# Kernel tuning notes

Measured on AMD Instinct MI355X. Metric: run time of the kernel, lower is better.

Reference implementation:

```python
import jax, jax.numpy as jnp
import numpy as np

B, M, T, N = 128, 256, 512, 512

def setup_inputs() -> dict:
    key = jax.random.key(0)
    ks = jax.random.split(key, 6)
    return {
        "hidden_state": jax.random.normal(ks[0], (B, M), jnp.float32),
        "cell_state": jax.random.normal(ks[1], (B, M), jnp.float32),
        "X": jax.random.normal(ks[2], (B, T, N), jnp.float32),
        "We1": jax.random.normal(ks[3], (2 * M, T), jnp.float32) * 0.05,
        "be1": jnp.zeros((T,), jnp.float32),
        "We2": jax.random.normal(ks[4], (T, T), jnp.float32) * 0.05,
        "be2": jnp.zeros((T,), jnp.float32),
        "v": jax.random.normal(ks[5], (T, 1), jnp.float32) * 0.05,
        "bv": jnp.zeros((1,), jnp.float32),
    }

def reference(hidden_state, cell_state, X, We1, be1, We2, be2, v, bv):
    # concat hidden + cell: [B, 2m]; Dense(T) then broadcast over n (K.repeat)
    hc = jnp.concatenate([hidden_state, cell_state], axis=-1)
    hs = (hc @ We1 + be1)[:, None, :]                 # [B, 1, T] (broadcast over n)
    # Permute X -> [B, n, T], Dense(T): contract over T
    ux = jnp.einsum('btn,tk->bnk', X, We2) + be2      # [B, n, T]
    # add + tanh + Dense(1) fused chain
    e = jnp.tanh(hs + ux) @ v + bv                    # [B, n, 1]
    # Permute -> [B, 1, n], softmax over last axis (n)
    attn = jax.nn.softmax(jnp.swapaxes(e, 1, 2), axis=-1)  # [B, 1, n]
    return attn
```

## Files before the change

kernel.cpp:

```cpp
#include <hip/hip_runtime.h>
#include <hip/hip_bf16.h>


typedef _Float16 half8 __attribute__((ext_vector_type(8)));
typedef float floatx4 __attribute__((ext_vector_type(4)));

__device__ __forceinline__ float fast_tanh(float x) {
    float cx = fminf(15.0f, fmaxf(-15.0f, x));
    float e = __expf(2.0f * cx);
    return (e - 1.0f) * __fdividef(1.0f, e + 1.0f);
}

__global__ __launch_bounds__(256) void k_prep_a(const float* __restrict__ We2,
                                                _Float16* __restrict__ Af) {
    __shared__ float w2[32][512];
    const int ts = blockIdx.x;
    for (int idx = threadIdx.x; idx < 32 * 512; idx += 256) {
        int tl = idx >> 9, k = idx & 511;
        w2[tl][k] = We2[(ts * 32 + tl) * 512 + k];
    }
    __syncthreads();
    for (int item = threadIdx.x; item < 32 * 64; item += 256) {
        int c = item >> 6, l = item & 63;
        int k  = c * 16 + (l & 15);
        int tl = (l >> 4) * 8;
        half8 h;
#pragma unroll
        for (int j = 0; j < 8; ++j) h[j] = (_Float16)w2[tl + j][k];
        *(half8*)&Af[(((size_t)ts * 32 + c) * 64 + l) * 8] = h;
    }
}

__global__ __launch_bounds__(256) void k_hs(const float* __restrict__ hidden,
                                            const float* __restrict__ cell,
                                            const float* __restrict__ We1,
                                            const float* __restrict__ be1,
                                            const float* __restrict__ be2,
                                            float* __restrict__ g) {
    __shared__ __align__(16) float hcl[8][512];
    __shared__ float red[4][8][64];
    const int b0 = (blockIdx.x >> 3) << 3;
    const int k0 = (blockIdx.x & 7) << 6;
    for (int idx = threadIdx.x; idx < 8 * 512; idx += 256) {
        int bi = idx >> 9, j = idx & 511;
        hcl[bi][j] = (j < 256) ? hidden[(b0 + bi) * 256 + j]
                               : cell[(b0 + bi) * 256 + j - 256];
    }
    __syncthreads();
    const int kl = threadIdx.x & 63;
    const int jc = threadIdx.x >> 6;
    const int k  = k0 + kl;
    float acc[8] = {};
    for (int j = jc * 128; j < jc * 128 + 128; j += 4) {
        float w0 = We1[(j + 0) * 512 + k];
        float w1 = We1[(j + 1) * 512 + k];
        float w2 = We1[(j + 2) * 512 + k];
        float w3 = We1[(j + 3) * 512 + k];
#pragma unroll
        for (int bi = 0; bi < 8; ++bi) {
            float4 h = *(const float4*)&hcl[bi][j];
            acc[bi] += h.x * w0 + h.y * w1 + h.z * w2 + h.w * w3;
        }
    }
#pragma unroll
    for (int bi = 0; bi < 8; ++bi) red[jc][bi][kl] = acc[bi];
    __syncthreads();
    for (int idx = threadIdx.x; idx < 512; idx += 256) {
        int bi = idx >> 6, kk = idx & 63;
        float s = red[0][bi][kk] + red[1][bi][kk] + red[2][bi][kk] + red[3][bi][kk];
        int kg = k0 + kk;
        g[(b0 + bi) * 512 + kg] = s + be1[kg] + be2[kg];
    }
}

__global__ __launch_bounds__(256, 3) void k_main(const float* __restrict__ X,
                                                 const _Float16* __restrict__ Af,
                                                 const float* __restrict__ g,
                                                 const float* __restrict__ vvec,
                                                 float* __restrict__ Ep) {
    __shared__ __align__(16) _Float16 Xb[2][2048];
    const int tid  = threadIdx.x;
    const int lane = tid & 63;
    const int wv   = tid >> 6;
    const int l16  = lane & 15;
    const int lhi  = lane >> 4;
    const int logical = (blockIdx.x & 7) * 256 + (blockIdx.x >> 3);
    const int kblk = logical & 1;
    const int nt   = (logical >> 1) & 7;
    const int b    = logical >> 4;
    const int n0   = nt << 6;

    const float* Xg = X + (size_t)b * 262144 + n0;
    const _Float16* Ag = Af + (size_t)(kblk * 16 + wv * 4) * 512 + (size_t)lane * 8;

    const int xn = tid & 63;
    const int xo = tid >> 6;
    const float* Xt = Xg + (size_t)(xo * 8) * 512 + xn;
    const int wslot = xn * 32 + ((xo ^ (xn & 3) ^ ((xn >> 2) & 3)) << 3);
    int roff[4];
#pragma unroll
    for (int nf = 0; nf < 4; ++nf) {
        int n = nf * 16 + l16;
        roff[nf] = n * 32 + ((lhi ^ (n & 3) ^ ((n >> 2) & 3)) << 3);
    }

    float xs0[8], xs1[8], xs2[8];
#define XLOAD(s_, arr_)                                                        \
    do { _Pragma("unroll")                                                     \
         for (int j = 0; j < 8; ++j)                                           \
             arr_[j] = Xt[(size_t)(s_) * 16384 + (size_t)j * 512];             \
    } while (0)
#define XSTORE(s_, arr_)                                                       \
    do { half8 h;                                                              \
         _Pragma("unroll")                                                     \
         for (int j = 0; j < 8; ++j) h[j] = (_Float16)arr_[j];                 \
         *(half8*)&Xb[(s_) & 1][wslot] = h;                                    \
    } while (0)

    XLOAD(0, xs0);
    XLOAD(1, xs1);
    XLOAD(2, xs2);
    XSTORE(0, xs0);
    asm volatile("s_waitcnt lgkmcnt(0)" ::: "memory");
    __builtin_amdgcn_sched_barrier(0);
    __builtin_amdgcn_s_barrier();
    __builtin_amdgcn_sched_barrier(0);

    floatx4 acc[4][4];
#pragma unroll
    for (int a = 0; a < 4; ++a)
#pragma unroll
        for (int c = 0; c < 4; ++c) acc[a][c] = (floatx4){0.f, 0.f, 0.f, 0.f};

#pragma unroll
    for (int s = 0; s < 16; ++s) {
        const int cur = s & 1;
        half8 af[4];
#pragma unroll
        for (int kf = 0; kf < 4; ++kf)
            af[kf] = *(const half8*)(Ag + (size_t)s * 16384 + (size_t)kf * 512);
        if (s + 3 < 16) {
            if ((s % 3) == 0)      XLOAD(s + 3, xs0);
            else if ((s % 3) == 1) XLOAD(s + 3, xs1);
            else                   XLOAD(s + 3, xs2);
        }
        half8 bf[4];
#pragma unroll
        for (int nf = 0; nf < 4; ++nf)
            bf[nf] = *(const half8*)&Xb[cur][roff[nf]];
        if (s + 1 < 16) {
            if (((s + 1) % 3) == 0)      XSTORE(s + 1, xs0);
            else if (((s + 1) % 3) == 1) XSTORE(s + 1, xs1);
            else                         XSTORE(s + 1, xs2);
        }
        __builtin_amdgcn_s_setprio(1);
#pragma unroll
        for (int kf = 0; kf < 4; ++kf)
#pragma unroll
            for (int nf = 0; nf < 4; ++nf)
                acc[kf][nf] = __builtin_amdgcn_mfma_f32_16x16x32_f16(
                    af[kf], bf[nf], acc[kf][nf], 0, 0, 0);
        __builtin_amdgcn_s_setprio(0);
        asm volatile("s_waitcnt lgkmcnt(0)" ::: "memory");
        __builtin_amdgcn_sched_barrier(0);
        __builtin_amdgcn_s_barrier();
        __builtin_amdgcn_sched_barrier(0);
    }
#undef XLOAD
#undef XSTORE

    const float* gb = g + b * 512;
    float sacc[4] = {0.f, 0.f, 0.f, 0.f};
#pragma unroll
    for (int kf = 0; kf < 4; ++kf) {
        const int kb = kblk * 256 + wv * 64 + kf * 16 + lhi * 4;
        float g0 = gb[kb + 0], g1 = gb[kb + 1], g2 = gb[kb + 2], g3 = gb[kb + 3];
        float v0 = vvec[kb + 0], v1 = vvec[kb + 1], v2 = vvec[kb + 2], v3 = vvec[kb + 3];
#pragma unroll
        for (int nf = 0; nf < 4; ++nf) {
            sacc[nf] += fast_tanh(acc[kf][nf][0] + g0) * v0;
            sacc[nf] += fast_tanh(acc[kf][nf][1] + g1) * v1;
            sacc[nf] += fast_tanh(acc[kf][nf][2] + g2) * v2;
            sacc[nf] += fast_tanh(acc[kf][nf][3] + g3) * v3;
        }
    }
#pragma unroll
    for (int nf = 0; nf < 4; ++nf) {
        sacc[nf] += __shfl_xor(sacc[nf], 16);
        sacc[nf] += __shfl_xor(sacc[nf], 32);
    }
    __syncthreads();
    float* ered = (float*)&Xb[0][0];
    if (lane < 16) {
#pragma unroll
        for (int nf = 0; nf < 4; ++nf) ered[wv * 64 + nf * 16 + l16] = sacc[nf];
    }
    __syncthreads();
    if (tid < 64) {
        float e = ered[tid] + ered[64 + tid] + ered[128 + tid] + ered[192 + tid];
        Ep[(size_t)kblk * 65536 + b * 512 + n0 + tid] = e;
    }
}

__global__ __launch_bounds__(256) void k_softmax(const float* __restrict__ Ep,
                                                 float* __restrict__ out) {
    __shared__ float rmax[4], rsum[4];
    const int b = blockIdx.x;
    const int tid = threadIdx.x;
    const float* E0 = Ep;
    const float* E1 = Ep + 65536;
    float e0 = E0[b * 512 + tid] + E1[b * 512 + tid];
    float e1 = E0[b * 512 + 256 + tid] + E1[b * 512 + 256 + tid];
    float m = fmaxf(e0, e1);
    for (int o = 32; o > 0; o >>= 1) m = fmaxf(m, __shfl_xor(m, o));
    if ((tid & 63) == 0) rmax[tid >> 6] = m;
    __syncthreads();
    m = fmaxf(fmaxf(rmax[0], rmax[1]), fmaxf(rmax[2], rmax[3]));
    float p0 = __expf(e0 - m), p1 = __expf(e1 - m);
    float ss = p0 + p1;
    for (int o = 32; o > 0; o >>= 1) ss += __shfl_xor(ss, o);
    if ((tid & 63) == 0) rsum[tid >> 6] = ss;
    __syncthreads();
    ss = rsum[0] + rsum[1] + rsum[2] + rsum[3];
    float inv = __fdividef(1.0f, ss);
    out[b * 512 + tid] = p0 * inv;
    out[b * 512 + 256 + tid] = p1 * inv;
}

extern "C" void kernel_launch(void* const* d_in, const int* in_sizes, int n_in,
                              void* d_out, int out_size, void* d_ws, size_t ws_size,
                              hipStream_t stream) {
    const float* hidden = (const float*)d_in[0];
    const float* cell   = (const float*)d_in[1];
    const float* X      = (const float*)d_in[2];
    const float* We1    = (const float*)d_in[3];
    const float* be1    = (const float*)d_in[4];
    const float* We2    = (const float*)d_in[5];
    const float* be2    = (const float*)d_in[6];
    const float* v      = (const float*)d_in[7];
    float* out = (float*)d_out;

    char* ws = (char*)d_ws;
    _Float16* Af = (_Float16*)ws;
    float* g     = (float*)(ws + 524288);
    float* Ep    = (float*)(ws + 786432);

    k_prep_a<<<16, 256, 0, stream>>>(We2, Af);
    k_hs<<<128, 256, 0, stream>>>(hidden, cell, We1, be1, be2, g);
    k_main<<<2048, 256, 0, stream>>>(X, Af, g, v, Ep);
    k_softmax<<<128, 256, 0, stream>>>(Ep, out);
}
```

Measured before the change: 78.42 us.

## Enlarge main GEMM tile to 128 rows with 8 waves and register-prefetched weights

Result: slower. 89.00 us (+13.5%).

```diff
diff --git a/kernel.cpp b/kernel.cpp
--- a/kernel.cpp
+++ b/kernel.cpp
@@ -73,54 +73,66 @@
     }
 }
 
-__global__ __launch_bounds__(256, 3) void k_main(const float* __restrict__ X,
+__global__ __launch_bounds__(512, 2) void k_main(const float* __restrict__ X,
                                                  const _Float16* __restrict__ Af,
                                                  const float* __restrict__ g,
                                                  const float* __restrict__ vvec,
                                                  float* __restrict__ Ep) {
-    __shared__ __align__(16) _Float16 Xb[2][2048];
+    __shared__ __align__(16) _Float16 Xb[2][8192];
     const int tid  = threadIdx.x;
     const int lane = tid & 63;
     const int wv   = tid >> 6;
     const int l16  = lane & 15;
     const int lhi  = lane >> 4;
-    const int logical = (blockIdx.x & 7) * 256 + (blockIdx.x >> 3);
+    const int mw   = wv >> 2;
+    const int kw   = wv & 3;
+    const int logical = (blockIdx.x & 7) * 128 + (blockIdx.x >> 3);
     const int kblk = logical & 1;
-    const int nt   = (logical >> 1) & 7;
-    const int b    = logical >> 4;
-    const int n0   = nt << 6;
+    const int nt   = (logical >> 1) & 3;
+    const int b    = logical >> 3;
+    const int n0   = nt << 7;
 
     const float* Xg = X + (size_t)b * 262144 + n0;
-    const _Float16* Ag = Af + (size_t)(kblk * 16 + wv * 4) * 512 + (size_t)lane * 8;
-
-    const int xn = tid & 63;
-    const int xo = tid >> 6;
-    const float* Xt = Xg + (size_t)(xo * 8) * 512 + xn;
-    const int wslot = xn * 32 + ((xo ^ (xn & 3) ^ ((xn >> 2) & 3)) << 3);
-    int roff[4];
-#pragma unroll
-    for (int nf = 0; nf < 4; ++nf) {
-        int n = nf * 16 + l16;
-        roff[nf] = n * 32 + ((lhi ^ (n & 3) ^ ((n >> 2) & 3)) << 3);
-    }
-
-    float xs0[8], xs1[8], xs2[8];
+    const _Float16* Ag = Af + (size_t)(kblk * 16 + kw * 4) * 512 + (size_t)lane * 8;
+
+    const int xn  = tid & 127;
+    const int xob = tid >> 7;
+    const float* Xt = Xg + (size_t)(xob * 8) * 512 + xn;
+    const int wsl0 = (((xn >> 4) * 2 + 0) * 64 + (xn & 15) + (xob << 4)) * 8;
+    const int wsl1 = (((xn >> 4) * 2 + 1) * 64 + (xn & 15) + (xob << 4)) * 8;
+
+    float xsA[16], xsB[16];
+    half8 wfA[8], wfB[8];
+
 #define XLOAD(s_, arr_)                                                        \
     do { _Pragma("unroll")                                                     \
-         for (int j = 0; j < 8; ++j)                                           \
-             arr_[j] = Xt[(size_t)(s_) * 16384 + (size_t)j * 512];             \
+         for (int r = 0; r < 2; ++r)                                           \
+             _Pragma("unroll")                                                 \
+             for (int j = 0; j < 8; ++j)                                       \
+                 arr_[r * 8 + j] =                                             \
+                     Xt[(size_t)((s_) * 64 + r * 32 + j) * 512];               \
     } while (0)
 #define XSTORE(s_, arr_)                                                       \
-    do { half8 h;                                                              \
+    do { half8 h0, h1;                                                         \
          _Pragma("unroll")                                                     \
-         for (int j = 0; j < 8; ++j) h[j] = (_Float16)arr_[j];                 \
-         *(half8*)&Xb[(s_) & 1][wslot] = h;                                    \
+         for (int j = 0; j < 8; ++j) { h0[j] = (_Float16)arr_[j];              \
+                                       h1[j] = (_Float16)arr_[8 + j]; }        \
+         *(half8*)&Xb[(s_) & 1][wsl0] = h0;                                    \
+         *(half8*)&Xb[(s_) & 1][wsl1] = h1;                                    \
     } while (0)
-
-    XLOAD(0, xs0);
-    XLOAD(1, xs1);
-    XLOAD(2, xs2);
-    XSTORE(0, xs0);
+#define WLOAD(s_, arr_)                                                        \
+    do { _Pragma("unroll")                                                     \
+         for (int ks = 0; ks < 2; ++ks)                                        \
+             _Pragma("unroll")                                                 \
+             for (int kf = 0; kf < 4; ++kf)                                    \
+                 arr_[ks * 4 + kf] = *(const half8*)                           \
+                     (Ag + (size_t)((s_) * 2 + ks) * 16384 + kf * 512);        \
+    } while (0)
+
+    XLOAD(0, xsA);
+    XLOAD(1, xsB);
+    WLOAD(0, wfA);
+    XSTORE(0, xsA);
     asm volatile("s_waitcnt lgkmcnt(0)" ::: "memory");
     __builtin_amdgcn_sched_barrier(0);
     __builtin_amdgcn_s_barrier();
@@ -133,33 +145,42 @@
         for (int c = 0; c < 4; ++c) acc[a][c] = (floatx4){0.f, 0.f, 0.f, 0.f};
 
 #pragma unroll
-    for (int s = 0; s < 16; ++s) {
+    for (int s = 0; s < 8; ++s) {
         const int cur = s & 1;
-        half8 af[4];
-#pragma unroll
-        for (int kf = 0; kf < 4; ++kf)
-            af[kf] = *(const half8*)(Ag + (size_t)s * 16384 + (size_t)kf * 512);
-        if (s + 3 < 16) {
-            if ((s % 3) == 0)      XLOAD(s + 3, xs0);
-            else if ((s % 3) == 1) XLOAD(s + 3, xs1);
-            else                   XLOAD(s + 3, xs2);
-        }
-        half8 bf[4];
-#pragma unroll
-        for (int nf = 0; nf < 4; ++nf)
-            bf[nf] = *(const half8*)&Xb[cur][roff[nf]];
-        if (s + 1 < 16) {
-            if (((s + 1) % 3) == 0)      XSTORE(s + 1, xs0);
-            else if (((s + 1) % 3) == 1) XSTORE(s + 1, xs1);
-            else                         XSTORE(s + 1, xs2);
-        }
+        if (s + 1 < 8) {
+            if ((s & 1) == 0) WLOAD(s + 1, wfB);
+            else              WLOAD(s + 1, wfA);
+        }
+        if (s + 2 < 8) {
+            if ((s & 1) == 0) XLOAD(s + 2, xsA);
+            else              XLOAD(s + 2, xsB);
+        }
+        __builtin_amdgcn_sched_barrier(0);
+        if (s + 1 < 8) {
+            if ((s & 1) == 0) XSTORE(s + 1, xsB);
+            else              XSTORE(s + 1, xsA);
+        }
+        __builtin_amdgcn_sched_barrier(0);
         __builtin_amdgcn_s_setprio(1);
 #pragma unroll
-        for (int kf = 0; kf < 4; ++kf)
-#pragma unroll
-            for (int nf = 0; nf < 4; ++nf)
-                acc[kf][nf] = __builtin_amdgcn_mfma_f32_16x16x32_f16(
-                    af[kf], bf[nf], acc[kf][nf], 0, 0, 0);
+        for (int mf = 0; mf < 4; ++mf) {
+#pragma unroll
+            for (int ks = 0; ks < 2; ++ks) {
+                half8 xf = *(const half8*)
+                    &Xb[cur][((mw * 4 + mf) * 2 + ks) * 512 + lane * 8];
+                if ((s & 1) == 0) {
+#pragma unroll
+                    for (int kf = 0; kf < 4; ++kf)
+                        acc[mf][kf] = __builtin_amdgcn_mfma_f32_16x16x32_f16(
+                            wfA[ks * 4 + kf], xf, acc[mf][kf], 0, 0, 0);
+                } else {
+#pragma unroll
+                    for (int kf = 0; kf < 4; ++kf)
+                        acc[mf][kf] = __builtin_amdgcn_mfma_f32_16x16x32_f16(
+                            wfB[ks * 4 + kf], xf, acc[mf][kf], 0, 0, 0);
+                }
+            }
+        }
         __builtin_amdgcn_s_setprio(0);
         asm volatile("s_waitcnt lgkmcnt(0)" ::: "memory");
         __builtin_amdgcn_sched_barrier(0);
@@ -168,36 +189,38 @@
     }
 #undef XLOAD
 #undef XSTORE
+#undef WLOAD
 
     const float* gb = g + b * 512;
     float sacc[4] = {0.f, 0.f, 0.f, 0.f};
 #pragma unroll
     for (int kf = 0; kf < 4; ++kf) {
-        const int kb = kblk * 256 + wv * 64 + kf * 16 + lhi * 4;
+        const int kb = kblk * 256 + kw * 64 + kf * 16 + lhi * 4;
         float g0 = gb[kb + 0], g1 = gb[kb + 1], g2 = gb[kb + 2], g3 = gb[kb + 3];
         float v0 = vvec[kb + 0], v1 = vvec[kb + 1], v2 = vvec[kb + 2], v3 = vvec[kb + 3];
 #pragma unroll
-        for (int nf = 0; nf < 4; ++nf) {
-            sacc[nf] += fast_tanh(acc[kf][nf][0] + g0) * v0;
-            sacc[nf] += fast_tanh(acc[kf][nf][1] + g1) * v1;
-            sacc[nf] += fast_tanh(acc[kf][nf][2] + g2) * v2;
-            sacc[nf] += fast_tanh(acc[kf][nf][3] + g3) * v3;
-        }
-    }
-#pragma unroll
-    for (int nf = 0; nf < 4; ++nf) {
-        sacc[nf] += __shfl_xor(sacc[nf], 16);
-        sacc[nf] += __shfl_xor(sacc[nf], 32);
+        for (int mf = 0; mf < 4; ++mf) {
+            sacc[mf] += fast_tanh(acc[mf][kf][0] + g0) * v0;
+            sacc[mf] += fast_tanh(acc[mf][kf][1] + g1) * v1;
+            sacc[mf] += fast_tanh(acc[mf][kf][2] + g2) * v2;
+            sacc[mf] += fast_tanh(acc[mf][kf][3] + g3) * v3;
+        }
+    }
+#pragma unroll
+    for (int mf = 0; mf < 4; ++mf) {
+        sacc[mf] += __shfl_xor(sacc[mf], 16);
+        sacc[mf] += __shfl_xor(sacc[mf], 32);
     }
     __syncthreads();
     float* ered = (float*)&Xb[0][0];
     if (lane < 16) {
 #pragma unroll
-        for (int nf = 0; nf < 4; ++nf) ered[wv * 64 + nf * 16 + l16] = sacc[nf];
-    }
-    __syncthreads();
-    if (tid < 64) {
-        float e = ered[tid] + ered[64 + tid] + ered[128 + tid] + ered[192 + tid];
+        for (int mf = 0; mf < 4; ++mf)
+            ered[kw * 128 + mw * 64 + mf * 16 + l16] = sacc[mf];
+    }
+    __syncthreads();
+    if (tid < 128) {
+        float e = ered[tid] + ered[128 + tid] + ered[256 + tid] + ered[384 + tid];
         Ep[(size_t)kblk * 65536 + b * 512 + n0 + tid] = e;
     }
 }
@@ -247,6 +270,6 @@
 
     k_prep_a<<<16, 256, 0, stream>>>(We2, Af);
     k_hs<<<128, 256, 0, stream>>>(hidden, cell, We1, be1, be2, g);
-    k_main<<<2048, 256, 0, stream>>>(X, Af, g, v, Ep);
+    k_main<<<1024, 512, 0, stream>>>(X, Af, g, v, Ep);
     k_softmax<<<128, 256, 0, stream>>>(Ep, out);
 }
```
